# Kernel tuning notes

Hardware: AMD Instinct MI355X
Metric: run time of the kernel (lower is better)

Reference implementation:

```python
import jax, jax.numpy as jnp
import numpy as np

N_NODES = 100000


def gcn_conv(x, edge_index, W, b):
    # GCNConv with add_self_loops=True, normalize=True (symmetric norm):
    # out = D^{-1/2} (A + I) D^{-1/2} (x @ W) + b
    n = x.shape[0]
    h = x @ W  # transform first (PyG applies lin before propagate)
    src, dst = edge_index[0], edge_index[1]
    ones = jnp.ones(src.shape[0], dtype=h.dtype)
    # degree with self-loops: in-degree + 1
    deg = jax.ops.segment_sum(ones, dst, num_segments=n) + 1.0
    dinv = jax.lax.rsqrt(deg)  # deg >= 1, always finite
    # per-edge normalized messages, scatter-add to dst
    msg = h[src] * (dinv[src] * dinv[dst])[:, None]
    agg = jax.ops.segment_sum(msg, dst, num_segments=n)
    # self-loop contribution: norm = dinv[i]^2
    agg = agg + h * (dinv * dinv)[:, None]
    return agg + b


def setup_inputs() -> dict:
    key = jax.random.key(0)
    ks = jax.random.split(key, 8)
    x = jax.random.normal(ks[0], (N_NODES, 256), dtype=jnp.float32)
    edge_index = jax.random.randint(ks[1], (2, 3200000), 0, N_NODES, dtype=jnp.int32)
    W1 = jax.random.normal(ks[2], (256, 32), dtype=jnp.float32) * (1.0 / np.sqrt(256))
    b1 = jnp.zeros((32,), dtype=jnp.float32)
    Wm = jax.random.normal(ks[3], (32, 16), dtype=jnp.float32) * (1.0 / np.sqrt(32))
    bm = jnp.zeros((16,), dtype=jnp.float32)
    Wv = jax.random.normal(ks[4], (32, 16), dtype=jnp.float32) * (1.0 / np.sqrt(32))
    bv = jnp.zeros((16,), dtype=jnp.float32)
    return {"x": x, "edge_index": edge_index, "W1": W1, "b1": b1,
            "Wm": Wm, "bm": bm, "Wv": Wv, "bv": bv}


def reference(x, edge_index, W1, b1, Wm, bm, Wv, bv):
    h = jax.nn.relu(gcn_conv(x, edge_index, W1, b1))
    mu = gcn_conv(h, edge_index, Wm, bm)
    sigma = gcn_conv(h, edge_index, Wv, bv)
    return (mu, sigma)
```

## Files before the change

kernel.cpp:

```cpp
#include <hip/hip_runtime.h>
#include <hip/hip_fp16.h>

#define NNODES 100000
#define NEDGES 3200000
#define F_IN   256
#define F_HID  32
#define F_OUT  16

#define NB   196
#define NPB  512
#define CAP  20480
#define NCHUNK 256
#define CHUNK  12500
#define RPT_B  20
#define RPT_A  13

#define GRID1 ((NNODES + 63) / 64)
#define XT_RS 130

typedef _Float16 half_t;
typedef half_t half8 __attribute__((ext_vector_type(8)));
typedef float f32x4 __attribute__((ext_vector_type(4)));
typedef const __attribute__((address_space(1))) unsigned int* gas_u32;
typedef __attribute__((address_space(3))) unsigned int* las_u32;


__global__ void k_init(int* __restrict__ bcur) {
    if (threadIdx.x < NB) bcur[threadIdx.x] = threadIdx.x * CAP;
}

__global__ __launch_bounds__(1024) void k_phaseA(
        const int* __restrict__ src, const int* __restrict__ dst,
        int* __restrict__ bcur, unsigned int* __restrict__ rec) {
    __shared__ int lh[NB];
    __shared__ int lcur[NB];
    int t = threadIdx.x;
    int e0 = blockIdx.x * CHUNK;
    if (t < NB) lh[t] = 0;

    int dcache[RPT_A];
    #pragma unroll
    for (int k = 0; k < RPT_A; ++k) {
        int i = t + k * 1024;
        dcache[k] = (i < CHUNK) ? dst[e0 + i] : -1;
    }
    __syncthreads();
    #pragma unroll
    for (int k = 0; k < RPT_A; ++k)
        if (dcache[k] >= 0) atomicAdd(&lh[dcache[k] >> 9], 1);
    __syncthreads();
    if (t < NB) lcur[t] = lh[t] ? atomicAdd(&bcur[t], lh[t]) : 0;
    __syncthreads();
    #pragma unroll
    for (int k = 0; k < RPT_A; ++k) {
        int i = t + k * 1024;
        if (dcache[k] >= 0) {
            int s = src[e0 + i];
            int d = dcache[k];
            int b = d >> 9;
            int pos = atomicAdd(&lcur[b], 1);
            rec[pos] = ((unsigned)s << 9) | (unsigned)(d & 511);
        }
    }
}

__global__ __launch_bounds__(1024) void k_phaseB(
        const unsigned int* __restrict__ rec, const int* __restrict__ bcur,
        int* __restrict__ rowptr, int* __restrict__ cnt,
        float* __restrict__ dinv, int* __restrict__ csr) {
    __shared__ int lh[NPB];
    __shared__ int lsc[NPB];
    __shared__ int wsum[16];
    int t = threadIdx.x, b = blockIdx.x;
    int lo = b * CAP;
    int nrec = bcur[b] - lo;
    if (t < NPB) lh[t] = 0;

    unsigned rcache[RPT_B];
    #pragma unroll
    for (int k = 0; k < RPT_B; ++k) {
        int i = t + k * 1024;
        rcache[k] = (i < nrec) ? rec[lo + i] : 0xFFFFFFFFu;
    }
    __syncthreads();
    #pragma unroll
    for (int k = 0; k < RPT_B; ++k)
        if (rcache[k] != 0xFFFFFFFFu) atomicAdd(&lh[rcache[k] & 511], 1);
    __syncthreads();

    int lane = t & 63, w = t >> 6;
    int my = (t < NPB) ? lh[t] : 0;
    int v = my;
    #pragma unroll
    for (int d = 1; d < 64; d <<= 1) {
        int tmp = __shfl_up(v, d, 64);
        if (lane >= d) v += tmp;
    }
    if (lane == 63) wsum[w] = v;
    __syncthreads();
    if (w == 0) {
        int s = (lane < 16) ? wsum[lane] : 0;
        #pragma unroll
        for (int d = 1; d < 16; d <<= 1) {
            int tmp = __shfl_up(s, d, 64);
            if (lane >= d) s += tmp;
        }
        if (lane < 16) wsum[lane] = s;
    }
    __syncthreads();
    int ex = v + (w > 0 ? wsum[w - 1] : 0) - my;
    int node = b * NPB + t;
    if (t < NPB) {
        lsc[t] = ex;
        if (node < NNODES) {
            rowptr[node] = lo + ex;
            cnt[node] = my;
            dinv[node] = rsqrtf((float)my + 1.0f);
        }
    }
    __syncthreads();
    #pragma unroll
    for (int k = 0; k < RPT_B; ++k)
        if (rcache[k] != 0xFFFFFFFFu) {
            int dl = rcache[k] & 511;
            int p = atomicAdd(&lsc[dl], 1);
            csr[lo + p] = (int)(rcache[k] >> 9);
        }
}


__global__ __launch_bounds__(256) void k_gemm1(
        const float* __restrict__ x, const float* __restrict__ W1,
        const float* __restrict__ dinv, __half2* __restrict__ g1) {
    __shared__ half_t Wt[32 * 264];
    __shared__ float xt[4][16 * XT_RS];
    int t = threadIdx.x;
    int wave = t >> 6, lane = t & 63;
    int m = lane & 15, q = lane >> 4;
    int row0 = blockIdx.x * 64 + wave * 16;

    for (int i = t; i < F_IN * F_HID; i += 256) {
        int k = i >> 5, f = i & 31;
        Wt[f * 264 + k] = (half_t)W1[i];
    }
    __syncthreads();

    half8 B[2][8];
    #pragma unroll
    for (int ft = 0; ft < 2; ++ft)
        #pragma unroll
        for (int kc = 0; kc < 8; ++kc)
            B[ft][kc] = *(const half8*)&Wt[(ft * 16 + m) * 264 + kc * 32 + q * 8];

    float* xw = xt[wave];
    f32x4 acc0 = {0.f, 0.f, 0.f, 0.f};
    f32x4 acc1 = {0.f, 0.f, 0.f, 0.f};
    #pragma unroll
    for (int kh = 0; kh < 2; ++kh) {
        #pragma unroll
        for (int r = 0; r < 16; ++r) {
            int grow = row0 + r; if (grow >= NNODES) grow = NNODES - 1;
            const float* gp = &x[(size_t)grow * F_IN + kh * 128 + lane];
            __builtin_amdgcn_global_load_lds((gas_u32)gp,
                (las_u32)&xw[r * XT_RS], 4, 0, 0);
        }
        #pragma unroll
        for (int r = 0; r < 16; ++r) {
            int grow = row0 + r; if (grow >= NNODES) grow = NNODES - 1;
            const float* gp = &x[(size_t)grow * F_IN + kh * 128 + lane];
            __builtin_amdgcn_global_load_lds((gas_u32)(gp + 64),
                (las_u32)&xw[r * XT_RS + 64], 4, 0, 0);
        }
        #pragma unroll
        for (int kc = 0; kc < 4; ++kc) {
            if (kc == 0) asm volatile("s_waitcnt vmcnt(16)" ::: "memory");
            if (kc == 2) asm volatile("s_waitcnt vmcnt(0)" ::: "memory");
            const float* sp = &xw[m * XT_RS + kc * 32 + q * 8];
            float2 x0 = *(const float2*)sp;
            float2 x1 = *(const float2*)(sp + 2);
            float2 x2 = *(const float2*)(sp + 4);
            float2 x3 = *(const float2*)(sp + 6);
            half8 A;
            A[0] = (half_t)x0.x; A[1] = (half_t)x0.y;
            A[2] = (half_t)x1.x; A[3] = (half_t)x1.y;
            A[4] = (half_t)x2.x; A[5] = (half_t)x2.y;
            A[6] = (half_t)x3.x; A[7] = (half_t)x3.y;
            acc0 = __builtin_amdgcn_mfma_f32_16x16x32_f16(A, B[0][kh * 4 + kc], acc0, 0, 0, 0);
            acc1 = __builtin_amdgcn_mfma_f32_16x16x32_f16(A, B[1][kh * 4 + kc], acc1, 0, 0, 0);
        }
        if (kh == 0) asm volatile("s_waitcnt lgkmcnt(0)" ::: "memory");
    }

    __syncthreads();
    float* sb = xw;
    #pragma unroll
    for (int r = 0; r < 4; ++r) {
        int rl = q * 4 + r;
        int grow = row0 + rl; if (grow >= NNODES) grow = NNODES - 1;
        float dv = dinv[grow];
        sb[rl * 33 + m]      = acc0[r] * dv;
        sb[rl * 33 + 16 + m] = acc1[r] * dv;
    }
    __syncthreads();
    int rl = (t >> 2) & 15;
    int w2 = t >> 6;
    int c0 = (t & 3) * 8;
    int grow = blockIdx.x * 64 + w2 * 16 + rl;
    if (grow < NNODES) {
        const float* sp = &xt[w2][rl * 33 + c0];
        __half2 h0 = __floats2half2_rn(sp[0], sp[1]);
        __half2 h1 = __floats2half2_rn(sp[2], sp[3]);
        __half2 h2 = __floats2half2_rn(sp[4], sp[5]);
        __half2 h3 = __floats2half2_rn(sp[6], sp[7]);
        __half2* gp = &g1[(size_t)grow * 16 + (c0 >> 1)];
        gp[0] = h0; gp[1] = h1; gp[2] = h2; gp[3] = h3;
    }
}


__global__ __launch_bounds__(256) void k_gather_l1(
        const int* __restrict__ rowptr, const int* __restrict__ cnt,
        const int* __restrict__ csr,
        const float* __restrict__ dinv, const __half2* __restrict__ g,
        const float* __restrict__ b1, const float* __restrict__ Wm,
        const float* __restrict__ Wv, __half2* __restrict__ g2) {
    __shared__ float Wcat[F_HID * 32];
    __shared__ float hrow[16][F_HID + 2];
    int tx = threadIdx.x;
    for (int idx = tx; idx < F_HID * 32; idx += 256) {
        int k = idx >> 5, j = idx & 31;
        Wcat[idx] = (j < F_OUT) ? Wm[k * F_OUT + j] : Wv[k * F_OUT + (j - F_OUT)];
    }
    int f2 = tx & 15;
    int lr = tx >> 4;
    int node = blockIdx.x * 16 + lr;
    int start = rowptr[node], end = start + cnt[node];
    float2 acc = __half22float2(g[(size_t)node * 16 + f2]);
    int j = start;
    for (; j + 4 <= end; j += 4) {
        int s0 = csr[j], s1 = csr[j + 1], s2 = csr[j + 2], s3 = csr[j + 3];
        float2 a0 = __half22float2(g[(size_t)s0 * 16 + f2]);
        float2 a1 = __half22float2(g[(size_t)s1 * 16 + f2]);
        float2 a2 = __half22float2(g[(size_t)s2 * 16 + f2]);
        float2 a3 = __half22float2(g[(size_t)s3 * 16 + f2]);
        acc.x += (a0.x + a1.x) + (a2.x + a3.x);
        acc.y += (a0.y + a1.y) + (a2.y + a3.y);
    }
    for (; j < end; ++j) {
        float2 a = __half22float2(g[(size_t)csr[j] * 16 + f2]);
        acc.x += a.x; acc.y += a.y;
    }
    float dv = dinv[node];
    float h0 = dv * acc.x + b1[2 * f2];
    float h1 = dv * acc.y + b1[2 * f2 + 1];
    hrow[lr][2 * f2]     = h0 > 0.f ? h0 : 0.f;
    hrow[lr][2 * f2 + 1] = h1 > 0.f ? h1 : 0.f;
    __syncthreads();
    float o0 = 0.f, o1 = 0.f;
    #pragma unroll
    for (int k = 0; k < F_HID; ++k) {
        float hv = hrow[lr][k];
        o0 = fmaf(hv, Wcat[k * 32 + 2 * f2], o0);
        o1 = fmaf(hv, Wcat[k * 32 + 2 * f2 + 1], o1);
    }
    g2[(size_t)node * 16 + f2] = __floats2half2_rn(o0 * dv, o1 * dv);
}


__global__ __launch_bounds__(256) void k_gather_out(
        const int* __restrict__ rowptr, const int* __restrict__ cnt,
        const int* __restrict__ csr,
        const float* __restrict__ dinv, const __half2* __restrict__ g,
        const float* __restrict__ bm, const float* __restrict__ bv,
        float* __restrict__ out) {
    int tx = threadIdx.x;
    int f2 = tx & 15;
    int node = blockIdx.x * 16 + (tx >> 4);
    int start = rowptr[node], end = start + cnt[node];
    float2 acc = __half22float2(g[(size_t)node * 16 + f2]);
    int j = start;
    for (; j + 4 <= end; j += 4) {
        int s0 = csr[j], s1 = csr[j + 1], s2 = csr[j + 2], s3 = csr[j + 3];
        float2 a0 = __half22float2(g[(size_t)s0 * 16 + f2]);
        float2 a1 = __half22float2(g[(size_t)s1 * 16 + f2]);
        float2 a2 = __half22float2(g[(size_t)s2 * 16 + f2]);
        float2 a3 = __half22float2(g[(size_t)s3 * 16 + f2]);
        acc.x += (a0.x + a1.x) + (a2.x + a3.x);
        acc.y += (a0.y + a1.y) + (a2.y + a3.y);
    }
    for (; j < end; ++j) {
        float2 a = __half22float2(g[(size_t)csr[j] * 16 + f2]);
        acc.x += a.x; acc.y += a.y;
    }
    float dv = dinv[node];
    int f = 2 * f2;
    if (f < F_OUT) {
        float2 o = { dv * acc.x + bm[f], dv * acc.y + bm[f + 1] };
        *(float2*)&out[(size_t)node * F_OUT + f] = o;
    } else {
        float2 o = { dv * acc.x + bv[f - F_OUT], dv * acc.y + bv[f - F_OUT + 1] };
        *(float2*)&out[(size_t)NNODES * F_OUT + (size_t)node * F_OUT + (f - F_OUT)] = o;
    }
}


extern "C" void kernel_launch(void* const* d_in, const int* in_sizes, int n_in,
                              void* d_out, int out_size, void* d_ws, size_t ws_size,
                              hipStream_t stream) {
    const float* x   = (const float*)d_in[0];
    const int*   ei  = (const int*)  d_in[1];
    const float* W1  = (const float*)d_in[2];
    const float* b1  = (const float*)d_in[3];
    const float* Wm  = (const float*)d_in[4];
    const float* bm  = (const float*)d_in[5];
    const float* Wv  = (const float*)d_in[6];
    const float* bv  = (const float*)d_in[7];
    float* out = (float*)d_out;

    const int* src = ei;
    const int* dst = ei + NEDGES;

    char* ws = (char*)d_ws;
    float*        dinv   = (float*)ws;        ws += 100352 * 4;
    int*          bcur   = (int*)ws;          ws += 256 * 4;
    int*          rowptr = (int*)ws;          ws += 100352 * 4;
    int*          cnt    = (int*)ws;          ws += 100352 * 4;
    int*          csr    = (int*)ws;          ws += (size_t)NB * CAP * 4;
    unsigned int* rec    = (unsigned int*)ws; ws += (size_t)NB * CAP * 4;
    __half2*      g2     = (__half2*)ws;

    __half2* g1 = (__half2*)rec;

    k_init  <<<1, 256, 0, stream>>>(bcur);
    k_phaseA<<<NCHUNK, 1024, 0, stream>>>(src, dst, bcur, rec);
    k_phaseB<<<NB, 1024, 0, stream>>>(rec, bcur, rowptr, cnt, dinv, csr);

    k_gemm1<<<GRID1, 256, 0, stream>>>(x, W1, dinv, g1);

    k_gather_l1<<<NNODES / 16, 256, 0, stream>>>(rowptr, cnt, csr, dinv, g1, b1, Wm, Wv, g2);

    k_gather_out<<<NNODES / 16, 256, 0, stream>>>(rowptr, cnt, csr, dinv, g2, bm, bv, out);
}
```

Measured before the change: 337.5 us.

## Load GEMM1 x rows directly to registers and unroll gathers by eight

The first GEMM no longer stages x tiles through LDS with async global-to-LDS loads and manual waitcnts. Each lane now reads its own float4 pairs straight from global memory into MFMA A operands, and the LDS buffer shrinks to a small output staging area. Both gather kernels gain an 8-way unrolled neighbor loop so more independent loads are in flight per thread. The risks are less coalesced x reads, with each lane touching 32-byte pieces of different rows, and higher register pressure in the gather kernels.

```diff
diff --git a/kernel.cpp b/kernel.cpp
--- a/kernel.cpp
+++ b/kernel.cpp
@@ -16,13 +16,10 @@
 #define RPT_A  13
 
 #define GRID1 ((NNODES + 63) / 64)
-#define XT_RS 130
 
 typedef _Float16 half_t;
 typedef half_t half8 __attribute__((ext_vector_type(8)));
 typedef float f32x4 __attribute__((ext_vector_type(4)));
-typedef const __attribute__((address_space(1))) unsigned int* gas_u32;
-typedef __attribute__((address_space(3))) unsigned int* las_u32;
 
 
 __global__ void k_init(int* __restrict__ bcur) {
@@ -133,7 +130,7 @@
         const float* __restrict__ x, const float* __restrict__ W1,
         const float* __restrict__ dinv, __half2* __restrict__ g1) {
     __shared__ half_t Wt[32 * 264];
-    __shared__ float xt[4][16 * XT_RS];
+    __shared__ float sb4[4][16 * 33];
     int t = threadIdx.x;
     int wave = t >> 6, lane = t & 63;
     int m = lane & 15, q = lane >> 4;
@@ -152,47 +149,26 @@
         for (int kc = 0; kc < 8; ++kc)
             B[ft][kc] = *(const half8*)&Wt[(ft * 16 + m) * 264 + kc * 32 + q * 8];
 
-    float* xw = xt[wave];
+    int grow_a = row0 + m; if (grow_a >= NNODES) grow_a = NNODES - 1;
+    const float* rowp = &x[(size_t)grow_a * F_IN + q * 8];
+
     f32x4 acc0 = {0.f, 0.f, 0.f, 0.f};
     f32x4 acc1 = {0.f, 0.f, 0.f, 0.f};
     #pragma unroll
-    for (int kh = 0; kh < 2; ++kh) {
-        #pragma unroll
-        for (int r = 0; r < 16; ++r) {
-            int grow = row0 + r; if (grow >= NNODES) grow = NNODES - 1;
-            const float* gp = &x[(size_t)grow * F_IN + kh * 128 + lane];
-            __builtin_amdgcn_global_load_lds((gas_u32)gp,
-                (las_u32)&xw[r * XT_RS], 4, 0, 0);
-        }
-        #pragma unroll
-        for (int r = 0; r < 16; ++r) {
-            int grow = row0 + r; if (grow >= NNODES) grow = NNODES - 1;
-            const float* gp = &x[(size_t)grow * F_IN + kh * 128 + lane];
-            __builtin_amdgcn_global_load_lds((gas_u32)(gp + 64),
-                (las_u32)&xw[r * XT_RS + 64], 4, 0, 0);
-        }
-        #pragma unroll
-        for (int kc = 0; kc < 4; ++kc) {
-            if (kc == 0) asm volatile("s_waitcnt vmcnt(16)" ::: "memory");
-            if (kc == 2) asm volatile("s_waitcnt vmcnt(0)" ::: "memory");
-            const float* sp = &xw[m * XT_RS + kc * 32 + q * 8];
-            float2 x0 = *(const float2*)sp;
-            float2 x1 = *(const float2*)(sp + 2);
-            float2 x2 = *(const float2*)(sp + 4);
-            float2 x3 = *(const float2*)(sp + 6);
-            half8 A;
-            A[0] = (half_t)x0.x; A[1] = (half_t)x0.y;
-            A[2] = (half_t)x1.x; A[3] = (half_t)x1.y;
-            A[4] = (half_t)x2.x; A[5] = (half_t)x2.y;
-            A[6] = (half_t)x3.x; A[7] = (half_t)x3.y;
-            acc0 = __builtin_amdgcn_mfma_f32_16x16x32_f16(A, B[0][kh * 4 + kc], acc0, 0, 0, 0);
-            acc1 = __builtin_amdgcn_mfma_f32_16x16x32_f16(A, B[1][kh * 4 + kc], acc1, 0, 0, 0);
-        }
-        if (kh == 0) asm volatile("s_waitcnt lgkmcnt(0)" ::: "memory");
-    }
-
-    __syncthreads();
-    float* sb = xw;
+    for (int kb = 0; kb < 8; ++kb) {
+        const float* sp = rowp + kb * 32;
+        float4 xa = *(const float4*)sp;
+        float4 xb = *(const float4*)(sp + 4);
+        half8 A;
+        A[0] = (half_t)xa.x; A[1] = (half_t)xa.y;
+        A[2] = (half_t)xa.z; A[3] = (half_t)xa.w;
+        A[4] = (half_t)xb.x; A[5] = (half_t)xb.y;
+        A[6] = (half_t)xb.z; A[7] = (half_t)xb.w;
+        acc0 = __builtin_amdgcn_mfma_f32_16x16x32_f16(A, B[0][kb], acc0, 0, 0, 0);
+        acc1 = __builtin_amdgcn_mfma_f32_16x16x32_f16(A, B[1][kb], acc1, 0, 0, 0);
+    }
+
+    float* sb = sb4[wave];
     #pragma unroll
     for (int r = 0; r < 4; ++r) {
         int rl = q * 4 + r;
@@ -207,7 +183,7 @@
     int c0 = (t & 3) * 8;
     int grow = blockIdx.x * 64 + w2 * 16 + rl;
     if (grow < NNODES) {
-        const float* sp = &xt[w2][rl * 33 + c0];
+        const float* sp = &sb4[w2][rl * 33 + c0];
         __half2 h0 = __floats2half2_rn(sp[0], sp[1]);
         __half2 h1 = __floats2half2_rn(sp[2], sp[3]);
         __half2 h2 = __floats2half2_rn(sp[4], sp[5]);
@@ -237,6 +213,18 @@
     int start = rowptr[node], end = start + cnt[node];
     float2 acc = __half22float2(g[(size_t)node * 16 + f2]);
     int j = start;
+    for (; j + 8 <= end; j += 8) {
+        int s[8];
+        #pragma unroll
+        for (int u = 0; u < 8; ++u) s[u] = csr[j + u];
+        float2 a[8];
+        #pragma unroll
+        for (int u = 0; u < 8; ++u) a[u] = __half22float2(g[(size_t)s[u] * 16 + f2]);
+        float sx = 0.f, sy = 0.f;
+        #pragma unroll
+        for (int u = 0; u < 8; ++u) { sx += a[u].x; sy += a[u].y; }
+        acc.x += sx; acc.y += sy;
+    }
     for (; j + 4 <= end; j += 4) {
         int s0 = csr[j], s1 = csr[j + 1], s2 = csr[j + 2], s3 = csr[j + 3];
         float2 a0 = __half22float2(g[(size_t)s0 * 16 + f2]);
@@ -279,6 +267,18 @@
     int start = rowptr[node], end = start + cnt[node];
     float2 acc = __half22float2(g[(size_t)node * 16 + f2]);
     int j = start;
+    for (; j + 8 <= end; j += 8) {
+        int s[8];
+        #pragma unroll
+        for (int u = 0; u < 8; ++u) s[u] = csr[j + u];
+        float2 a[8];
+        #pragma unroll
+        for (int u = 0; u < 8; ++u) a[u] = __half22float2(g[(size_t)s[u] * 16 + f2]);
+        float sx = 0.f, sy = 0.f;
+        #pragma unroll
+        for (int u = 0; u < 8; ++u) { sx += a[u].x; sy += a[u].y; }
+        acc.x += sx; acc.y += sy;
+    }
     for (; j + 4 <= end; j += 4) {
         int s0 = csr[j], s1 = csr[j + 1], s2 = csr[j + 2], s3 = csr[j + 3];
         float2 a0 = __half22float2(g[(size_t)s0 * 16 + f2]);
```

After: 320.7 us. 5.0% less time.
